# Kernel tuning notes

Hardware: AMD Instinct MI355X
Metric: run time of the kernel (lower is better)

Reference implementation:

```python
import jax, jax.numpy as jnp
import numpy as np

N_NODES = 100000
N_EDGES = 600000
EMB = 128
L = 5
NUM_ATOM = 119
NUM_CHIR = 3
NUM_BTYPE = 5
NUM_BDIR = 3
BN_EPS = 1e-5


def setup_inputs() -> dict:
    key = jax.random.key(0)
    ks = jax.random.split(key, 16)
    inp = {}
    inp['x'] = jax.random.randint(ks[0], (N_NODES, 2), 0, NUM_ATOM, dtype=jnp.int64 if jax.config.jax_enable_x64 else jnp.int32)
    inp['edge_index'] = jax.random.randint(ks[1], (2, N_EDGES), 0, N_NODES)
    inp['edge_attr'] = jax.random.randint(ks[2], (N_EDGES, 2), 0, NUM_BDIR)
    s = 0.05
    inp['x_emb1'] = jax.random.normal(ks[3], (NUM_ATOM, EMB), jnp.float32) * s
    inp['x_emb2'] = jax.random.normal(ks[4], (NUM_CHIR, EMB), jnp.float32) * s
    inp['edge_emb1'] = jax.random.normal(ks[5], (L, NUM_BTYPE, EMB), jnp.float32) * s
    inp['edge_emb2'] = jax.random.normal(ks[6], (L, NUM_BDIR, EMB), jnp.float32) * s
    inp['W1'] = jax.random.normal(ks[7], (L, EMB, 2 * EMB), jnp.float32) * (1.0 / np.sqrt(EMB))
    inp['b1'] = jnp.zeros((L, 2 * EMB), jnp.float32)
    inp['W2'] = jax.random.normal(ks[8], (L, 2 * EMB, EMB), jnp.float32) * (1.0 / np.sqrt(2 * EMB))
    inp['b2'] = jnp.zeros((L, EMB), jnp.float32)
    inp['eps'] = jnp.zeros((L,), jnp.float32)
    inp['gamma'] = jnp.ones((L, EMB), jnp.float32)
    inp['beta'] = jnp.zeros((L, EMB), jnp.float32)
    return inp


def reference(x, edge_index, edge_attr, x_emb1, x_emb2, edge_emb1, edge_emb2,
              W1, b1, W2, b2, eps, gamma, beta):
    N = x.shape[0]
    # node embedding: sum of two table lookups
    x0 = jnp.clip(x[:, 0], 0, x_emb1.shape[0] - 1)
    x1 = jnp.clip(x[:, 1], 0, x_emb2.shape[0] - 1)
    h = x_emb1[x0] + x_emb2[x1]  # [N, EMB]
    # add self loops (loop edge_attr = zeros -> bond type 0 / dir 0)
    loop = jnp.arange(N, dtype=edge_index.dtype)
    src = jnp.concatenate([edge_index[0], loop])  # [E+N]
    dst = jnp.concatenate([edge_index[1], loop])
    ea = jnp.concatenate([edge_attr, jnp.zeros((N, 2), dtype=edge_attr.dtype)], axis=0)
    e0 = jnp.clip(ea[:, 0], 0, edge_emb1.shape[1] - 1)
    e1 = jnp.clip(ea[:, 1], 0, edge_emb2.shape[1] - 1)
    n_layers = eps.shape[0]
    for i in range(n_layers):
        e = edge_emb1[i][e0] + edge_emb2[i][e1]              # [E+N, EMB]
        m = jax.nn.relu(h[src] + e)                           # gather + elementwise
        agg = jax.ops.segment_sum(m, dst, num_segments=N)     # scatter-add
        out = (1.0 + eps[i]) * h + agg
        # MLP: Linear -> ReLU -> Linear
        hmid = jax.nn.relu(out @ W1[i] + b1[i])
        h = hmid @ W2[i] + b2[i]
        # BatchNorm1d over nodes (batch statistics, biased variance)
        mean = jnp.mean(h, axis=0)
        var = jnp.mean((h - mean) ** 2, axis=0)
        h = (h - mean) * jax.lax.rsqrt(var + BN_EPS) * gamma[i] + beta[i]
        if i < n_layers - 1:
            h = jax.nn.relu(h)
    return h
```

## Files before the change

### kernel.cpp

```cpp
#include <hip/hip_runtime.h>

#define NN 100000
#define NPAD 100096
#define NE 600000
#define EMB 128

typedef unsigned short u16;
typedef unsigned int u32;
typedef _Float16 half8 __attribute__((ext_vector_type(8)));
typedef float f32x4 __attribute__((ext_vector_type(4)));

__device__ __forceinline__ float4 ld4(const float* p) { return *(const float4*)p; }
__device__ __forceinline__ u32 packh2(float a, float b) {
  union { _Float16 h[2]; u32 d; } u;
  u.h[0] = (_Float16)a;
  u.h[1] = (_Float16)b;
  return u.d;
}

__global__ __launch_bounds__(256) void node_init_kernel(
    const int* __restrict__ x, const float* __restrict__ emb1,
    const float* __restrict__ emb2, _Float16* __restrict__ hb) {
  int tid = blockIdx.x * blockDim.x + threadIdx.x;
  int n = tid >> 4;
  if (n >= NN) return;
  int kc = tid & 15;
  int x0 = min(max(x[2 * n], 0), 118);
  int x1 = min(max(x[2 * n + 1], 0), 2);
  const float* p1 = emb1 + (size_t)x0 * EMB + kc * 8;
  const float* p2 = emb2 + (size_t)x1 * EMB + kc * 8;
  _Float16 o[8];
#pragma unroll
  for (int j = 0; j < 8; ++j) o[j] = (_Float16)(p1[j] + p2[j]);
  *(ulonglong2*)(hb + (size_t)n * EMB + kc * 8) = *(ulonglong2*)o;
}

__global__ __launch_bounds__(256) void hist_kernel(const int* __restrict__ ei,
                                                   int* __restrict__ deg) {
  int e = blockIdx.x * blockDim.x + threadIdx.x;
  if (e >= NE) return;
  atomicAdd(&deg[ei[NE + e]], 1);
}

__global__ __launch_bounds__(256) void scan1_kernel(const int* __restrict__ deg,
                                                    int* __restrict__ off,
                                                    int* __restrict__ bsum) {
  __shared__ int s[256];
  int t = threadIdx.x;
  int base = blockIdx.x * 1024 + t * 4;
  int v[4];
#pragma unroll
  for (int j = 0; j < 4; ++j) {
    int idx = base + j;
    v[j] = (idx < NN) ? deg[idx] : 0;
  }
  int tsum = v[0] + v[1] + v[2] + v[3];
  s[t] = tsum;
  __syncthreads();
  for (int d = 1; d < 256; d <<= 1) {
    int add = (t >= d) ? s[t - d] : 0;
    __syncthreads();
    s[t] += add;
    __syncthreads();
  }
  int run = s[t] - tsum;
#pragma unroll
  for (int j = 0; j < 4; ++j) {
    int idx = base + j;
    if (idx < NN) off[idx] = run;
    run += v[j];
  }
  if (t == 255) bsum[blockIdx.x] = s[255];
}

__global__ void scan2_kernel(int* __restrict__ bsum, int* __restrict__ off, int nb) {
  if (threadIdx.x == 0) {
    int run = 0;
    for (int b = 0; b < nb; ++b) {
      int v = bsum[b];
      bsum[b] = run;
      run += v;
    }
    off[NN] = run;
  }
}

__global__ __launch_bounds__(256) void scan3_kernel(int* __restrict__ off,
                                                    const int* __restrict__ bsum) {
  int idx = blockIdx.x * blockDim.x + threadIdx.x;
  if (idx < NN) off[idx] += bsum[idx >> 10];
}

__global__ __launch_bounds__(256) void scatter_kernel(
    const int* __restrict__ ei, const int* __restrict__ ea,
    const int* __restrict__ off, int* __restrict__ cnt, int* __restrict__ csr) {
  int e = blockIdx.x * blockDim.x + threadIdx.x;
  if (e >= NE) return;
  int d = ei[NE + e];
  int s = ei[e];
  int a0 = min(max(ea[2 * e], 0), 4);
  int a1 = min(max(ea[2 * e + 1], 0), 2);
  int code = a0 * 3 + a1;
  int r = atomicAdd(&cnt[d], 1);
  csr[off[d] + r] = s | (code << 20);
}

__global__ __launch_bounds__(256) void combo_kernel(const float* __restrict__ ee1,
                                                    const float* __restrict__ ee2,
                                                    float* __restrict__ combos) {
  int idx = blockIdx.x * blockDim.x + threadIdx.x;
  if (idx >= 5 * 15 * 128) return;
  int l = idx / (15 * 128);
  int rem = idx % (15 * 128);
  int code = rem / 128;
  int f = rem % 128;
  combos[idx] = ee1[(l * 5 + code / 3) * 128 + f] + ee2[(l * 3 + code % 3) * 128 + f];
}

__global__ __launch_bounds__(256) void prep_w_kernel(
    const float* __restrict__ W1g, const float* __restrict__ W2g,
    _Float16* __restrict__ W1f, _Float16* __restrict__ W2f) {
  int idx = blockIdx.x * blockDim.x + threadIdx.x;
  if (idx >= 40960) return;
  _Float16 o[8];
  if (idx < 20480) {
    int lane = idx & 63;
    int r = idx >> 6;
    int nt = r & 3, kt = (r >> 2) & 3, c = (r >> 4) & 3, l = r >> 6;
    int n = c * 64 + nt * 16 + (lane & 15);
    int kb = kt * 32 + (lane >> 4) * 8;
#pragma unroll
    for (int j = 0; j < 8; ++j) o[j] = (_Float16)W1g[((size_t)l * 128 + kb + j) * 256 + n];
    *(ulonglong2*)(W1f + (size_t)idx * 8) = *(ulonglong2*)o;
  } else {
    int i2 = idx - 20480;
    int lane = i2 & 63;
    int r = i2 >> 6;
    int nt = r & 7, ktl = (r >> 3) & 1, c = (r >> 4) & 3, l = r >> 6;
    int n = nt * 16 + (lane & 15);
    int kb = c * 64 + ktl * 32 + (lane >> 4) * 8;
#pragma unroll
    for (int j = 0; j < 8; ++j) o[j] = (_Float16)W2g[((size_t)l * 256 + kb + j) * 128 + n];
    *(ulonglong2*)(W2f + (size_t)i2 * 8) = *(ulonglong2*)o;
  }
}

__global__ __launch_bounds__(256) void agg_kernel(
    const _Float16* __restrict__ hb, const int* __restrict__ off,
    const int* __restrict__ csr, const float* __restrict__ cb,
    const float* __restrict__ epsp, _Float16* __restrict__ Af) {
  int tid = blockIdx.x * blockDim.x + threadIdx.x;
  int g = tid >> 4;
  int kc = tid & 15;
  float av[8] = {0.f, 0.f, 0.f, 0.f, 0.f, 0.f, 0.f, 0.f};
  if (g < NN) {
    const float eps1 = 1.0f + *epsp;
    ulonglong2 hraw = *(const ulonglong2*)(hb + (size_t)g * EMB + kc * 8);
    _Float16* hr = (_Float16*)&hraw;
    float4 ca = ld4(cb + kc * 8), cbv = ld4(cb + kc * 8 + 4);
    float cs[8] = {ca.x, ca.y, ca.z, ca.w, cbv.x, cbv.y, cbv.z, cbv.w};
#pragma unroll
    for (int j = 0; j < 8; ++j) {
      float hv = (float)hr[j];
      av[j] = eps1 * hv + fmaxf(hv + cs[j], 0.f);
    }
    int s0 = off[g], s1 = off[g + 1];
    int e = s0;
    for (; e + 1 < s1; e += 2) {
      int p0 = csr[e], p1 = csr[e + 1];
      ulonglong2 r0 = *(const ulonglong2*)(hb + (size_t)(p0 & 0xFFFFF) * EMB + kc * 8);
      ulonglong2 r1 = *(const ulonglong2*)(hb + (size_t)(p1 & 0xFFFFF) * EMB + kc * 8);
      const float* c0p = cb + (size_t)(p0 >> 20) * EMB + kc * 8;
      const float* c1p = cb + (size_t)(p1 >> 20) * EMB + kc * 8;
      float4 c0a = ld4(c0p), c0b = ld4(c0p + 4);
      float4 c1a = ld4(c1p), c1b = ld4(c1p + 4);
      float cc0[8] = {c0a.x, c0a.y, c0a.z, c0a.w, c0b.x, c0b.y, c0b.z, c0b.w};
      float cc1[8] = {c1a.x, c1a.y, c1a.z, c1a.w, c1b.x, c1b.y, c1b.z, c1b.w};
      _Float16* s0p = (_Float16*)&r0;
      _Float16* s1p = (_Float16*)&r1;
#pragma unroll
      for (int j = 0; j < 8; ++j) {
        av[j] += fmaxf((float)s0p[j] + cc0[j], 0.f);
        av[j] += fmaxf((float)s1p[j] + cc1[j], 0.f);
      }
    }
    if (e < s1) {
      int p0 = csr[e];
      ulonglong2 r0 = *(const ulonglong2*)(hb + (size_t)(p0 & 0xFFFFF) * EMB + kc * 8);
      const float* c0p = cb + (size_t)(p0 >> 20) * EMB + kc * 8;
      float4 c0a = ld4(c0p), c0b = ld4(c0p + 4);
      float cc0[8] = {c0a.x, c0a.y, c0a.z, c0a.w, c0b.x, c0b.y, c0b.z, c0b.w};
      _Float16* s0p = (_Float16*)&r0;
#pragma unroll
      for (int j = 0; j < 8; ++j) av[j] += fmaxf((float)s0p[j] + cc0[j], 0.f);
    }
  }
  _Float16 o[8];
#pragma unroll
  for (int j = 0; j < 8; ++j) o[j] = (_Float16)av[j];
  *(ulonglong2*)(Af + (size_t)g * EMB + kc * 8) = *(ulonglong2*)o;
}

__global__ __launch_bounds__(256, 4) void mlp_kernel(
    const _Float16* __restrict__ Af, const _Float16* __restrict__ W1f,
    const _Float16* __restrict__ W2f,
    const float* __restrict__ b1g, const float* __restrict__ b2g,
    float* __restrict__ hpre, float* __restrict__ slots) {
  __shared__ __align__(16) _Float16 Ws[16 * 64 * 8];

  const int t = threadIdx.x;
  const int w = t >> 6;
  const int lane = t & 63;
  const int q = lane >> 4, l15 = lane & 15;
  const int gw = blockIdx.x * 4 + w;
  const int n0 = gw * 16;
  float* sums = slots + (size_t)(gw & 31) * 256;

  half8 nh[4];
#pragma unroll
  for (int kt = 0; kt < 4; ++kt)
    nh[kt] = *(const half8*)(Af + (size_t)(n0 + l15) * EMB + kt * 32 + q * 8);

  f32x4 oacc[8];
#pragma unroll
  for (int a = 0; a < 8; ++a) oacc[a] = (f32x4){0.f, 0.f, 0.f, 0.f};

  const int srcA = ((q & 1) * 2) * 16 + l15;
  const int srcB = srcA + 16;
  const bool sel = (q >> 1) != 0;

  for (int c = 0; c < 4; ++c) {
    __syncthreads();
    {
      const _Float16* gb = W1f + ((size_t)(c * 16 + w * 4) * 64 + lane) * 8;
#pragma unroll
      for (int j = 0; j < 4; ++j)
        *(ulonglong2*)&Ws[(w * 4 + j) * 512 + lane * 8] =
            *(const ulonglong2*)(gb + (size_t)j * 512);
    }
    __syncthreads();

    f32x4 hacc[4];
#pragma unroll
    for (int a = 0; a < 4; ++a) hacc[a] = (f32x4){0.f, 0.f, 0.f, 0.f};
#pragma unroll
    for (int kt = 0; kt < 4; ++kt) {
#pragma unroll
      for (int colt = 0; colt < 4; ++colt) {
        half8 wh = *(const half8*)&Ws[(kt * 4 + colt) * 512 + lane * 8];
        hacc[colt] = __builtin_amdgcn_mfma_f32_16x16x32_f16(wh, nh[kt], hacc[colt], 0, 0, 0);
      }
    }
    __syncthreads();

    {
      const _Float16* gb = W2f + ((size_t)(c * 16 + w * 4) * 64 + lane) * 8;
#pragma unroll
      for (int j = 0; j < 4; ++j)
        *(ulonglong2*)&Ws[(w * 4 + j) * 512 + lane * 8] =
            *(const ulonglong2*)(gb + (size_t)j * 512);
    }

    u32 P01[4], P23[4];
#pragma unroll
    for (int colt = 0; colt < 4; ++colt) {
      float4 b1v = ld4(b1g + c * 64 + colt * 16 + q * 4);
      float v0 = fmaxf(hacc[colt][0] + b1v.x, 0.f);
      float v1 = fmaxf(hacc[colt][1] + b1v.y, 0.f);
      float v2 = fmaxf(hacc[colt][2] + b1v.z, 0.f);
      float v3 = fmaxf(hacc[colt][3] + b1v.w, 0.f);
      P01[colt] = packh2(v0, v1);
      P23[colt] = packh2(v2, v3);
    }
    __syncthreads();

#pragma unroll
    for (int ktl = 0; ktl < 2; ++ktl) {
      half8 bh;
      {
        union { u32 d[4]; half8 s; } uh;
        int c0 = 2 * ktl, c1 = 2 * ktl + 1;
        u32 a0, a1;
        a0 = (u32)__shfl((int)P01[c0], srcA); a1 = (u32)__shfl((int)P01[c1], srcA);
        uh.d[0] = sel ? a1 : a0;
        a0 = (u32)__shfl((int)P23[c0], srcA); a1 = (u32)__shfl((int)P23[c1], srcA);
        uh.d[1] = sel ? a1 : a0;
        a0 = (u32)__shfl((int)P01[c0], srcB); a1 = (u32)__shfl((int)P01[c1], srcB);
        uh.d[2] = sel ? a1 : a0;
        a0 = (u32)__shfl((int)P23[c0], srcB); a1 = (u32)__shfl((int)P23[c1], srcB);
        uh.d[3] = sel ? a1 : a0;
        bh = uh.s;
      }
#pragma unroll
      for (int nt = 0; nt < 8; ++nt) {
        half8 wh = *(const half8*)&Ws[(ktl * 8 + nt) * 512 + lane * 8];
        oacc[nt] = __builtin_amdgcn_mfma_f32_16x16x32_f16(wh, bh, oacc[nt], 0, 0, 0);
      }
    }
  }

  const int node = n0 + l15;
#pragma unroll
  for (int nt = 0; nt < 8; ++nt) {
    int ocb = nt * 16 + q * 4;
    float4 b2v = ld4(b2g + ocb);
    f32x4 s = (f32x4){0.f, 0.f, 0.f, 0.f};
    f32x4 s2 = (f32x4){0.f, 0.f, 0.f, 0.f};
    if (node < NN) {
      float4 v;
      v.x = oacc[nt][0] + b2v.x;
      v.y = oacc[nt][1] + b2v.y;
      v.z = oacc[nt][2] + b2v.z;
      v.w = oacc[nt][3] + b2v.w;
      *(float4*)(hpre + (size_t)node * EMB + ocb) = v;
      s[0] = v.x; s[1] = v.y; s[2] = v.z; s[3] = v.w;
      s2[0] = v.x * v.x; s2[1] = v.y * v.y; s2[2] = v.z * v.z; s2[3] = v.w * v.w;
    }
#pragma unroll
    for (int d = 1; d < 16; d <<= 1) {
#pragma unroll
      for (int r = 0; r < 4; ++r) {
        s[r] += __shfl_xor(s[r], d);
        s2[r] += __shfl_xor(s2[r], d);
      }
    }
    if (l15 == 0) {
#pragma unroll
      for (int r = 0; r < 4; ++r) {
        atomicAdd(&sums[ocb + r], s[r]);
        atomicAdd(&sums[128 + ocb + r], s2[r]);
      }
    }
  }
}

template <bool LAST>
__global__ __launch_bounds__(256) void bn_apply_kernel(
    const float* __restrict__ hp, const float* __restrict__ slots,
    const float* __restrict__ gamma, const float* __restrict__ beta,
    _Float16* __restrict__ hb, float* __restrict__ out) {
  __shared__ float ssc[128], ssh[128];
  int t = threadIdx.x;
  if (t < 128) {
    float s = 0.f, s2 = 0.f;
#pragma unroll 8
    for (int k = 0; k < 32; ++k) {
      s += slots[k * 256 + t];
      s2 += slots[k * 256 + 128 + t];
    }
    float mean = s * (1.0f / NN);
    float var = s2 * (1.0f / NN) - mean * mean;
    float sc = gamma[t] * rsqrtf(var + 1e-5f);
    ssc[t] = sc;
    ssh[t] = beta[t] - mean * sc;
  }
  __syncthreads();
  int tid = blockIdx.x * blockDim.x + t;
  int n = tid >> 4;
  if (n >= NN) return;
  int kc = tid & 15;
  const float* p = hp + (size_t)n * EMB + kc * 8;
  float4 va = ld4(p), vb = ld4(p + 4);
  float v[8] = {va.x, va.y, va.z, va.w, vb.x, vb.y, vb.z, vb.w};
#pragma unroll
  for (int j = 0; j < 8; ++j) v[j] = v[j] * ssc[kc * 8 + j] + ssh[kc * 8 + j];
  if (LAST) {
    float* d = out + (size_t)n * EMB + kc * 8;
    *(float4*)d = make_float4(v[0], v[1], v[2], v[3]);
    *(float4*)(d + 4) = make_float4(v[4], v[5], v[6], v[7]);
  } else {
    _Float16 o[8];
#pragma unroll
    for (int j = 0; j < 8; ++j) o[j] = (_Float16)fmaxf(v[j], 0.f);
    *(ulonglong2*)(hb + (size_t)n * EMB + kc * 8) = *(ulonglong2*)o;
  }
}

extern "C" void kernel_launch(void* const* d_in, const int* in_sizes, int n_in,
                              void* d_out, int out_size, void* d_ws, size_t ws_size,
                              hipStream_t stream) {
  const int* x = (const int*)d_in[0];
  const int* ei = (const int*)d_in[1];
  const int* ea = (const int*)d_in[2];
  const float* x_emb1 = (const float*)d_in[3];
  const float* x_emb2 = (const float*)d_in[4];
  const float* ee1 = (const float*)d_in[5];
  const float* ee2 = (const float*)d_in[6];
  const float* W1 = (const float*)d_in[7];
  const float* b1 = (const float*)d_in[8];
  const float* W2 = (const float*)d_in[9];
  const float* b2 = (const float*)d_in[10];
  const float* eps = (const float*)d_in[11];
  const float* gamma = (const float*)d_in[12];
  const float* beta = (const float*)d_in[13];
  float* out = (float*)d_out;

  float* hpre = (float*)d_ws;
  float* slots = hpre + (size_t)NN * EMB;
  float* combos = slots + 5 * 32 * 256;
  _Float16* Af = (_Float16*)(combos + 9600);
  _Float16* hb = Af + (size_t)NPAD * EMB;
  _Float16* W1f = hb + (size_t)NN * EMB;
  _Float16* W2f = W1f + 5 * 32768;
  int* deg = (int*)(W2f + 5 * 32768);
  int* off = deg + NN;
  int* csr = off + NN + 1;
  int* bsum = csr + NE;

  const int NB_SCAN = (NN + 1023) / 1024;

  hipMemsetAsync(deg, 0, NN * sizeof(int), stream);
  hipMemsetAsync(slots, 0, 5 * 32 * 256 * sizeof(float), stream);
  hist_kernel<<<(NE + 255) / 256, 256, 0, stream>>>(ei, deg);
  scan1_kernel<<<NB_SCAN, 256, 0, stream>>>(deg, off, bsum);
  scan2_kernel<<<1, 64, 0, stream>>>(bsum, off, NB_SCAN);
  scan3_kernel<<<(NN + 255) / 256, 256, 0, stream>>>(off, bsum);
  hipMemsetAsync(deg, 0, NN * sizeof(int), stream);
  scatter_kernel<<<(NE + 255) / 256, 256, 0, stream>>>(ei, ea, off, deg, csr);
  combo_kernel<<<(5 * 15 * 128 + 255) / 256, 256, 0, stream>>>(ee1, ee2, combos);
  prep_w_kernel<<<160, 256, 0, stream>>>(W1, W2, W1f, W2f);
  node_init_kernel<<<NN * 16 / 256 + 1, 256, 0, stream>>>(x, x_emb1, x_emb2, hb);

  const int NBLK = NPAD / 64;
  for (int i = 0; i < 5; ++i) {
    agg_kernel<<<NPAD * 16 / 256, 256, 0, stream>>>(
        hb, off, csr, combos + (size_t)i * 15 * EMB, eps + i, Af);
    mlp_kernel<<<NBLK, 256, 0, stream>>>(
        Af, W1f + (size_t)i * 32768, W2f + (size_t)i * 32768,
        b1 + (size_t)i * 256, b2 + (size_t)i * 128, hpre,
        slots + (size_t)i * 32 * 256);
    if (i < 4)
      bn_apply_kernel<false><<<NN * 16 / 256 + 1, 256, 0, stream>>>(
          hpre, slots + (size_t)i * 32 * 256, gamma + (size_t)i * EMB,
          beta + (size_t)i * EMB, hb, nullptr);
    else
      bn_apply_kernel<true><<<NN * 16 / 256 + 1, 256, 0, stream>>>(
          hpre, slots + (size_t)i * 32 * 256, gamma + (size_t)i * EMB,
          beta + (size_t)i * EMB, nullptr, out);
  }
}
```

Before: 694.3 us.

## Fuse BatchNorm apply into next layer's gather and store pre-BN activations in fp16

The per-layer BN-apply pass is removed. A tiny stats kernel now computes per-feature scale and shift, and the next layer's aggregation kernel applies normalization and ReLU on the fly to every gathered neighbour row. Pre-BN activations are stored as fp16 instead of fp32, which halves that write traffic. The MLP kernel loads W1 and W2 tiles together into a doubled shared buffer and drops two barriers. The gather loop is unrolled by four. The trade-off is redundant scale/shift arithmetic per edge (about 7x per node) and fp16 rounding of pre-BN values, which can affect accuracy.

After: 692.2 us. About the same (-0.3%).

```diff
diff --git a/kernel.cpp b/kernel.cpp
--- a/kernel.cpp
+++ b/kernel.cpp
@@ -7,6 +7,7 @@
 
 typedef unsigned short u16;
 typedef unsigned int u32;
+typedef unsigned long long u64;
 typedef _Float16 half8 __attribute__((ext_vector_type(8)));
 typedef float f32x4 __attribute__((ext_vector_type(4)));
 
@@ -145,54 +146,74 @@
   }
 }
 
+template <bool NORM>
 __global__ __launch_bounds__(256) void agg_kernel(
-    const _Float16* __restrict__ hb, const int* __restrict__ off,
-    const int* __restrict__ csr, const float* __restrict__ cb,
-    const float* __restrict__ epsp, _Float16* __restrict__ Af) {
+    const _Float16* __restrict__ hsrc, const float* __restrict__ scsh,
+    const int* __restrict__ off, const int* __restrict__ csr,
+    const float* __restrict__ cb, const float* __restrict__ epsp,
+    _Float16* __restrict__ Af) {
   int tid = blockIdx.x * blockDim.x + threadIdx.x;
   int g = tid >> 4;
   int kc = tid & 15;
   float av[8] = {0.f, 0.f, 0.f, 0.f, 0.f, 0.f, 0.f, 0.f};
+  float scv[8], shv[8];
+  if (NORM) {
+    float4 sa = ld4(scsh + kc * 8), sb = ld4(scsh + kc * 8 + 4);
+    float4 ha = ld4(scsh + 128 + kc * 8), hbv = ld4(scsh + 128 + kc * 8 + 4);
+    scv[0] = sa.x; scv[1] = sa.y; scv[2] = sa.z; scv[3] = sa.w;
+    scv[4] = sb.x; scv[5] = sb.y; scv[6] = sb.z; scv[7] = sb.w;
+    shv[0] = ha.x; shv[1] = ha.y; shv[2] = ha.z; shv[3] = ha.w;
+    shv[4] = hbv.x; shv[5] = hbv.y; shv[6] = hbv.z; shv[7] = hbv.w;
+  }
   if (g < NN) {
     const float eps1 = 1.0f + *epsp;
-    ulonglong2 hraw = *(const ulonglong2*)(hb + (size_t)g * EMB + kc * 8);
+    ulonglong2 hraw = *(const ulonglong2*)(hsrc + (size_t)g * EMB + kc * 8);
     _Float16* hr = (_Float16*)&hraw;
     float4 ca = ld4(cb + kc * 8), cbv = ld4(cb + kc * 8 + 4);
     float cs[8] = {ca.x, ca.y, ca.z, ca.w, cbv.x, cbv.y, cbv.z, cbv.w};
 #pragma unroll
     for (int j = 0; j < 8; ++j) {
       float hv = (float)hr[j];
+      if (NORM) hv = fmaxf(hv * scv[j] + shv[j], 0.f);
       av[j] = eps1 * hv + fmaxf(hv + cs[j], 0.f);
     }
     int s0 = off[g], s1 = off[g + 1];
     int e = s0;
-    for (; e + 1 < s1; e += 2) {
-      int p0 = csr[e], p1 = csr[e + 1];
-      ulonglong2 r0 = *(const ulonglong2*)(hb + (size_t)(p0 & 0xFFFFF) * EMB + kc * 8);
-      ulonglong2 r1 = *(const ulonglong2*)(hb + (size_t)(p1 & 0xFFFFF) * EMB + kc * 8);
-      const float* c0p = cb + (size_t)(p0 >> 20) * EMB + kc * 8;
-      const float* c1p = cb + (size_t)(p1 >> 20) * EMB + kc * 8;
-      float4 c0a = ld4(c0p), c0b = ld4(c0p + 4);
-      float4 c1a = ld4(c1p), c1b = ld4(c1p + 4);
-      float cc0[8] = {c0a.x, c0a.y, c0a.z, c0a.w, c0b.x, c0b.y, c0b.z, c0b.w};
-      float cc1[8] = {c1a.x, c1a.y, c1a.z, c1a.w, c1b.x, c1b.y, c1b.z, c1b.w};
-      _Float16* s0p = (_Float16*)&r0;
-      _Float16* s1p = (_Float16*)&r1;
+    for (; e + 3 < s1; e += 4) {
+      int p0 = csr[e], p1 = csr[e + 1], p2 = csr[e + 2], p3 = csr[e + 3];
+      ulonglong2 r0 = *(const ulonglong2*)(hsrc + (size_t)(p0 & 0xFFFFF) * EMB + kc * 8);
+      ulonglong2 r1 = *(const ulonglong2*)(hsrc + (size_t)(p1 & 0xFFFFF) * EMB + kc * 8);
+      ulonglong2 r2 = *(const ulonglong2*)(hsrc + (size_t)(p2 & 0xFFFFF) * EMB + kc * 8);
+      ulonglong2 r3 = *(const ulonglong2*)(hsrc + (size_t)(p3 & 0xFFFFF) * EMB + kc * 8);
+      ulonglong2 rr[4] = {r0, r1, r2, r3};
+      int pp[4] = {p0, p1, p2, p3};
+#pragma unroll
+      for (int u = 0; u < 4; ++u) {
+        const float* cp = cb + (size_t)(pp[u] >> 20) * EMB + kc * 8;
+        float4 c0 = ld4(cp), c1 = ld4(cp + 4);
+        float cc[8] = {c0.x, c0.y, c0.z, c0.w, c1.x, c1.y, c1.z, c1.w};
+        _Float16* sp = (_Float16*)&rr[u];
+#pragma unroll
+        for (int j = 0; j < 8; ++j) {
+          float v = (float)sp[j];
+          if (NORM) v = fmaxf(v * scv[j] + shv[j], 0.f);
+          av[j] += fmaxf(v + cc[j], 0.f);
+        }
+      }
+    }
+    for (; e < s1; ++e) {
+      int p0 = csr[e];
+      ulonglong2 r0 = *(const ulonglong2*)(hsrc + (size_t)(p0 & 0xFFFFF) * EMB + kc * 8);
+      const float* cp = cb + (size_t)(p0 >> 20) * EMB + kc * 8;
+      float4 c0 = ld4(cp), c1 = ld4(cp + 4);
+      float cc[8] = {c0.x, c0.y, c0.z, c0.w, c1.x, c1.y, c1.z, c1.w};
+      _Float16* sp = (_Float16*)&r0;
 #pragma unroll
       for (int j = 0; j < 8; ++j) {
-        av[j] += fmaxf((float)s0p[j] + cc0[j], 0.f);
-        av[j] += fmaxf((float)s1p[j] + cc1[j], 0.f);
-      }
-    }
-    if (e < s1) {
-      int p0 = csr[e];
-      ulonglong2 r0 = *(const ulonglong2*)(hb + (size_t)(p0 & 0xFFFFF) * EMB + kc * 8);
-      const float* c0p = cb + (size_t)(p0 >> 20) * EMB + kc * 8;
-      float4 c0a = ld4(c0p), c0b = ld4(c0p + 4);
-      float cc0[8] = {c0a.x, c0a.y, c0a.z, c0a.w, c0b.x, c0b.y, c0b.z, c0b.w};
-      _Float16* s0p = (_Float16*)&r0;
-#pragma unroll
-      for (int j = 0; j < 8; ++j) av[j] += fmaxf((float)s0p[j] + cc0[j], 0.f);
+        float v = (float)sp[j];
+        if (NORM) v = fmaxf(v * scv[j] + shv[j], 0.f);
+        av[j] += fmaxf(v + cc[j], 0.f);
+      }
     }
   }
   _Float16 o[8];
@@ -205,8 +226,8 @@
     const _Float16* __restrict__ Af, const _Float16* __restrict__ W1f,
     const _Float16* __restrict__ W2f,
     const float* __restrict__ b1g, const float* __restrict__ b2g,
-    float* __restrict__ hpre, float* __restrict__ slots) {
-  __shared__ __align__(16) _Float16 Ws[16 * 64 * 8];
+    _Float16* __restrict__ hpre, float* __restrict__ slots) {
+  __shared__ __align__(16) _Float16 Ws[2 * 16 * 64 * 8];
 
   const int t = threadIdx.x;
   const int w = t >> 6;
@@ -232,11 +253,15 @@
   for (int c = 0; c < 4; ++c) {
     __syncthreads();
     {
-      const _Float16* gb = W1f + ((size_t)(c * 16 + w * 4) * 64 + lane) * 8;
-#pragma unroll
-      for (int j = 0; j < 4; ++j)
+      const _Float16* g1 = W1f + ((size_t)(c * 16 + w * 4) * 64 + lane) * 8;
+      const _Float16* g2 = W2f + ((size_t)(c * 16 + w * 4) * 64 + lane) * 8;
+#pragma unroll
+      for (int j = 0; j < 4; ++j) {
         *(ulonglong2*)&Ws[(w * 4 + j) * 512 + lane * 8] =
-            *(const ulonglong2*)(gb + (size_t)j * 512);
+            *(const ulonglong2*)(g1 + (size_t)j * 512);
+        *(ulonglong2*)&Ws[8192 + (w * 4 + j) * 512 + lane * 8] =
+            *(const ulonglong2*)(g2 + (size_t)j * 512);
+      }
     }
     __syncthreads();
 
@@ -250,15 +275,6 @@
         half8 wh = *(const half8*)&Ws[(kt * 4 + colt) * 512 + lane * 8];
         hacc[colt] = __builtin_amdgcn_mfma_f32_16x16x32_f16(wh, nh[kt], hacc[colt], 0, 0, 0);
       }
-    }
-    __syncthreads();
-
-    {
-      const _Float16* gb = W2f + ((size_t)(c * 16 + w * 4) * 64 + lane) * 8;
-#pragma unroll
-      for (int j = 0; j < 4; ++j)
-        *(ulonglong2*)&Ws[(w * 4 + j) * 512 + lane * 8] =
-            *(const ulonglong2*)(gb + (size_t)j * 512);
     }
 
     u32 P01[4], P23[4];
@@ -272,7 +288,6 @@
       P01[colt] = packh2(v0, v1);
       P23[colt] = packh2(v2, v3);
     }
-    __syncthreads();
 
 #pragma unroll
     for (int ktl = 0; ktl < 2; ++ktl) {
@@ -293,7 +308,7 @@
       }
 #pragma unroll
       for (int nt = 0; nt < 8; ++nt) {
-        half8 wh = *(const half8*)&Ws[(ktl * 8 + nt) * 512 + lane * 8];
+        half8 wh = *(const half8*)&Ws[8192 + (ktl * 8 + nt) * 512 + lane * 8];
         oacc[nt] = __builtin_amdgcn_mfma_f32_16x16x32_f16(wh, bh, oacc[nt], 0, 0, 0);
       }
     }
@@ -307,14 +322,14 @@
     f32x4 s = (f32x4){0.f, 0.f, 0.f, 0.f};
     f32x4 s2 = (f32x4){0.f, 0.f, 0.f, 0.f};
     if (node < NN) {
-      float4 v;
-      v.x = oacc[nt][0] + b2v.x;
-      v.y = oacc[nt][1] + b2v.y;
-      v.z = oacc[nt][2] + b2v.z;
-      v.w = oacc[nt][3] + b2v.w;
-      *(float4*)(hpre + (size_t)node * EMB + ocb) = v;
-      s[0] = v.x; s[1] = v.y; s[2] = v.z; s[3] = v.w;
-      s2[0] = v.x * v.x; s2[1] = v.y * v.y; s2[2] = v.z * v.z; s2[3] = v.w * v.w;
+      float v0 = oacc[nt][0] + b2v.x;
+      float v1 = oacc[nt][1] + b2v.y;
+      float v2 = oacc[nt][2] + b2v.z;
+      float v3 = oacc[nt][3] + b2v.w;
+      u64 pk = (u64)packh2(v0, v1) | ((u64)packh2(v2, v3) << 32);
+      *(u64*)(hpre + (size_t)node * EMB + ocb) = pk;
+      s[0] = v0; s[1] = v1; s[2] = v2; s[3] = v3;
+      s2[0] = v0 * v0; s2[1] = v1 * v1; s2[2] = v2 * v2; s2[3] = v3 * v3;
     }
 #pragma unroll
     for (int d = 1; d < 16; d <<= 1) {
@@ -334,46 +349,43 @@
   }
 }
 
-template <bool LAST>
-__global__ __launch_bounds__(256) void bn_apply_kernel(
-    const float* __restrict__ hp, const float* __restrict__ slots,
-    const float* __restrict__ gamma, const float* __restrict__ beta,
-    _Float16* __restrict__ hb, float* __restrict__ out) {
-  __shared__ float ssc[128], ssh[128];
-  int t = threadIdx.x;
-  if (t < 128) {
-    float s = 0.f, s2 = 0.f;
+__global__ void stats_kernel(const float* __restrict__ slots,
+                             const float* __restrict__ gamma,
+                             const float* __restrict__ beta,
+                             float* __restrict__ scsh) {
+  int f = threadIdx.x;
+  float s = 0.f, s2 = 0.f;
 #pragma unroll 8
-    for (int k = 0; k < 32; ++k) {
-      s += slots[k * 256 + t];
-      s2 += slots[k * 256 + 128 + t];
-    }
-    float mean = s * (1.0f / NN);
-    float var = s2 * (1.0f / NN) - mean * mean;
-    float sc = gamma[t] * rsqrtf(var + 1e-5f);
-    ssc[t] = sc;
-    ssh[t] = beta[t] - mean * sc;
-  }
-  __syncthreads();
-  int tid = blockIdx.x * blockDim.x + t;
+  for (int k = 0; k < 32; ++k) {
+    s += slots[k * 256 + f];
+    s2 += slots[k * 256 + 128 + f];
+  }
+  float mean = s * (1.0f / NN);
+  float var = s2 * (1.0f / NN) - mean * mean;
+  float sc = gamma[f] * rsqrtf(var + 1e-5f);
+  scsh[f] = sc;
+  scsh[128 + f] = beta[f] - mean * sc;
+}
+
+__global__ __launch_bounds__(256) void out_kernel(
+    const _Float16* __restrict__ hpre, const float* __restrict__ scsh,
+    float* __restrict__ out) {
+  int tid = blockIdx.x * blockDim.x + threadIdx.x;
   int n = tid >> 4;
   if (n >= NN) return;
   int kc = tid & 15;
-  const float* p = hp + (size_t)n * EMB + kc * 8;
-  float4 va = ld4(p), vb = ld4(p + 4);
-  float v[8] = {va.x, va.y, va.z, va.w, vb.x, vb.y, vb.z, vb.w};
-#pragma unroll
-  for (int j = 0; j < 8; ++j) v[j] = v[j] * ssc[kc * 8 + j] + ssh[kc * 8 + j];
-  if (LAST) {
-    float* d = out + (size_t)n * EMB + kc * 8;
-    *(float4*)d = make_float4(v[0], v[1], v[2], v[3]);
-    *(float4*)(d + 4) = make_float4(v[4], v[5], v[6], v[7]);
-  } else {
-    _Float16 o[8];
-#pragma unroll
-    for (int j = 0; j < 8; ++j) o[j] = (_Float16)fmaxf(v[j], 0.f);
-    *(ulonglong2*)(hb + (size_t)n * EMB + kc * 8) = *(ulonglong2*)o;
-  }
+  ulonglong2 raw = *(const ulonglong2*)(hpre + (size_t)n * EMB + kc * 8);
+  _Float16* hr = (_Float16*)&raw;
+  float4 sa = ld4(scsh + kc * 8), sb = ld4(scsh + kc * 8 + 4);
+  float4 ha = ld4(scsh + 128 + kc * 8), hbv = ld4(scsh + 128 + kc * 8 + 4);
+  float scv[8] = {sa.x, sa.y, sa.z, sa.w, sb.x, sb.y, sb.z, sb.w};
+  float shv[8] = {ha.x, ha.y, ha.z, ha.w, hbv.x, hbv.y, hbv.z, hbv.w};
+  float v[8];
+#pragma unroll
+  for (int j = 0; j < 8; ++j) v[j] = (float)hr[j] * scv[j] + shv[j];
+  float* d = out + (size_t)n * EMB + kc * 8;
+  *(float4*)d = make_float4(v[0], v[1], v[2], v[3]);
+  *(float4*)(d + 4) = make_float4(v[4], v[5], v[6], v[7]);
 }
 
 extern "C" void kernel_launch(void* const* d_in, const int* in_sizes, int n_in,
@@ -395,10 +407,11 @@
   const float* beta = (const float*)d_in[13];
   float* out = (float*)d_out;
 
-  float* hpre = (float*)d_ws;
-  float* slots = hpre + (size_t)NN * EMB;
-  float* combos = slots + 5 * 32 * 256;
-  _Float16* Af = (_Float16*)(combos + 9600);
+  float* slots = (float*)d_ws;
+  float* scsh = slots + 5 * 32 * 256;
+  float* combos = scsh + 5 * 256;
+  _Float16* hpre = (_Float16*)(combos + 9600);
+  _Float16* Af = hpre + (size_t)NN * EMB;
   _Float16* hb = Af + (size_t)NPAD * EMB;
   _Float16* W1f = hb + (size_t)NN * EMB;
   _Float16* W2f = W1f + 5 * 32768;
@@ -423,19 +436,21 @@
 
   const int NBLK = NPAD / 64;
   for (int i = 0; i < 5; ++i) {
-    agg_kernel<<<NPAD * 16 / 256, 256, 0, stream>>>(
-        hb, off, csr, combos + (size_t)i * 15 * EMB, eps + i, Af);
+    if (i == 0)
+      agg_kernel<false><<<NPAD * 16 / 256, 256, 0, stream>>>(
+          hb, nullptr, off, csr, combos + (size_t)i * 15 * EMB, eps + i, Af);
+    else
+      agg_kernel<true><<<NPAD * 16 / 256, 256, 0, stream>>>(
+          hpre, scsh + (size_t)(i - 1) * 256, off, csr,
+          combos + (size_t)i * 15 * EMB, eps + i, Af);
     mlp_kernel<<<NBLK, 256, 0, stream>>>(
         Af, W1f + (size_t)i * 32768, W2f + (size_t)i * 32768,
         b1 + (size_t)i * 256, b2 + (size_t)i * 128, hpre,
         slots + (size_t)i * 32 * 256);
-    if (i < 4)
-      bn_apply_kernel<false><<<NN * 16 / 256 + 1, 256, 0, stream>>>(
-          hpre, slots + (size_t)i * 32 * 256, gamma + (size_t)i * EMB,
-          beta + (size_t)i * EMB, hb, nullptr);
-    else
-      bn_apply_kernel<true><<<NN * 16 / 256 + 1, 256, 0, stream>>>(
-          hpre, slots + (size_t)i * 32 * 256, gamma + (size_t)i * EMB,
-          beta + (size_t)i * EMB, nullptr, out);
-  }
-}
+    stats_kernel<<<1, 128, 0, stream>>>(slots + (size_t)i * 32 * 256,
+                                        gamma + (size_t)i * EMB,
+                                        beta + (size_t)i * EMB,
+                                        scsh + (size_t)i * 256);
+  }
+  out_kernel<<<NN * 16 / 256 + 1, 256, 0, stream>>>(hpre, scsh + 4 * 256, out);
+}
```
